# Performance work log

Hardware: AMD Instinct MI355X
Metric: run time of the kernel (lower is better)

Reference implementation:

```python
import jax, jax.numpy as jnp
import numpy as np

N_NODES = 10000
N_EDGES = 320000
D_FEAT = 128          # per-node feature dim -> in_dim = 2*D_FEAT = 256
OUT_DIM = 128
SCALES = 3


def setup_inputs() -> dict:
    key = jax.random.key(0)
    ks = jax.random.split(key, 7)
    node_features = jax.random.normal(ks[0], (N_NODES, D_FEAT), dtype=jnp.float32)
    temporal_info = jax.random.normal(ks[1], (N_NODES,), dtype=jnp.float32)
    in_dim_p1 = 2 * D_FEAT + 1  # 257: concat(src, dest) + temporal gap
    W1 = jax.random.normal(ks[2], (SCALES, in_dim_p1, OUT_DIM), dtype=jnp.float32) * 0.05
    b1 = jax.random.normal(ks[3], (SCALES, OUT_DIM), dtype=jnp.float32) * 0.05
    W2 = jax.random.normal(ks[4], (SCALES, OUT_DIM, OUT_DIM), dtype=jnp.float32) * 0.05
    b2 = jax.random.normal(ks[5], (SCALES, OUT_DIM), dtype=jnp.float32) * 0.05
    edge_index = jax.random.randint(ks[6], (2, N_EDGES), 0, N_NODES, dtype=jnp.int64)
    return {
        "node_features": node_features,
        "temporal_info": temporal_info,
        "W1": W1, "b1": b1, "W2": W2, "b2": b2,
        "edge_index": edge_index,
    }


def reference(node_features, temporal_info, W1, b1, W2, b2, edge_index):
    src, dest = edge_index[0], edge_index[1]
    # gather node pairs + temporal gap -> [E, 2*D+1]
    gap = (temporal_info[src] - temporal_info[dest])[:, None]
    edge_features = jnp.concatenate(
        [node_features[src], node_features[dest], gap], axis=-1)
    # all scales' 2-layer MLPs in one batched einsum; s = scale axis
    h = jax.nn.relu(jnp.einsum('ef,sfo->seo', edge_features, W1) + b1[:, None, :])
    tokens = jnp.einsum('seo,sop->sep', h, W2) + b2[:, None, :]  # [S, E, OUT]
    return tokens.mean(axis=0)  # mean over scales -> [E, OUT]
```

## Files before the change

kernel.cpp:

```cpp
#include <hip/hip_runtime.h>
#include <stdint.h>

#define NN 10000
#define NE 320000
#define DF 128
#define OD 128
#define NS 3

typedef __attribute__((ext_vector_type(8))) short bf16x8;
typedef __attribute__((ext_vector_type(16))) float f32x16;

static __device__ __forceinline__ uint32_t f2bf(float f) {
  uint32_t u = __float_as_uint(f);
  return (u + 0x7FFFu + ((u >> 16) & 1u)) >> 16;
}
static __device__ __forceinline__ float bflo(uint32_t u) { return __uint_as_float(u << 16); }
static __device__ __forceinline__ float bfhi(uint32_t u) { return __uint_as_float(u & 0xFFFF0000u); }

static __device__ __forceinline__ uint32_t relu2(uint32_t a, uint32_t d) {
  float f0 = fmaxf(bflo(a) + bflo(d), 0.0f);
  float f1 = fmaxf(bfhi(a) + bfhi(d), 0.0f);
  return f2bf(f0) | (f2bf(f1) << 16);
}

static __device__ __forceinline__ void lds_barrier() {
  asm volatile("s_waitcnt lgkmcnt(0)" ::: "memory");
  __builtin_amdgcn_s_barrier();
}

__global__ __launch_bounds__(256) void prep_w2(
    const float* __restrict__ W2, const float* __restrict__ b2,
    unsigned short* __restrict__ w2t, float* __restrict__ bmean)
{
  int tid = blockIdx.x * 256 + threadIdx.x;
  if (tid < NS * OD * OD) {
    int s = tid / (OD * OD);
    int r = tid % (OD * OD);
    int k = r / OD;
    int n = r % OD;
    w2t[(s * OD + n) * OD + k] = (unsigned short)f2bf(W2[tid]);
  }
  if (tid < OD) bmean[tid] = (b2[tid] + b2[OD + tid] + b2[2 * OD + tid]) * (1.0f / 3.0f);
}

__global__ __launch_bounds__(256) void node_proj(
    const float* __restrict__ nf, const float* __restrict__ temporal,
    const float* __restrict__ W1, const float* __restrict__ b1,
    unsigned short* __restrict__ Qsrc, unsigned short* __restrict__ Qdst)
{
  __shared__ unsigned short Asm[8 * 64 * 8];
  __shared__ unsigned short Bsm[4 * 8 * 64 * 8];
  __shared__ float tsh[32];

  const int t = threadIdx.x;
  const int c = blockIdx.y;
  const int s = c >> 1, proj = c & 1;

  {
    int o = t & 127, qh = t >> 7;
    const float* wbase = W1 + (size_t)(s * 257 + proj * 128) * OD + o;
    int nt = o >> 5, lnlo = o & 31;
    #pragma unroll
    for (int r = 0; r < 8; r++) {
      int kh = qh * 8 + r;
      float v[8];
      #pragma unroll
      for (int j = 0; j < 8; j++) v[j] = wbase[(size_t)(kh * 8 + j) * OD];
      uint32_t pk[4];
      #pragma unroll
      for (int i = 0; i < 4; i++) pk[i] = f2bf(v[2 * i]) | (f2bf(v[2 * i + 1]) << 16);
      int q = kh >> 1, half = kh & 1;
      uint32_t* d = (uint32_t*)(Bsm + ((nt * 8 + q) * 64 + half * 32 + lnlo) * 8);
      d[0] = pk[0]; d[1] = pk[1]; d[2] = pk[2]; d[3] = pk[3];
    }
  }

  const int lane = t & 63, w = t >> 6;
  const int o = w * 32 + (lane & 31);
  const float w1gv = W1[(size_t)(s * 257 + 256) * OD + o];
  const float b1v = b1[s * OD + o];
  unsigned short* Qt = (proj == 0) ? Qsrc : Qdst;
  const int m = t >> 3, j16 = t & 7;

  for (int it = 0; it < 8; it++) {
    const int m0 = (blockIdx.x * 8 + it) * 32;
    if (m0 >= NN) break;

    if (t < 32) tsh[t] = (m0 + t < NN) ? temporal[m0 + t] : 0.0f;

    {
      int node = m0 + m;
      float v[16];
      if (node < NN) {
        const float4* p = (const float4*)(nf + (size_t)node * DF + j16 * 16);
        #pragma unroll
        for (int i = 0; i < 4; i++) {
          float4 x = p[i];
          v[4 * i] = x.x; v[4 * i + 1] = x.y; v[4 * i + 2] = x.z; v[4 * i + 3] = x.w;
        }
      } else {
        #pragma unroll
        for (int i = 0; i < 16; i++) v[i] = 0.0f;
      }
      uint32_t pk[8];
      #pragma unroll
      for (int i = 0; i < 8; i++) pk[i] = f2bf(v[2 * i]) | (f2bf(v[2 * i + 1]) << 16);
      uint32_t* d0 = (uint32_t*)(Asm + (j16 * 64 + (m ^ j16)) * 8);
      uint32_t* d1 = (uint32_t*)(Asm + (j16 * 64 + ((32 + m) ^ j16)) * 8);
      d0[0] = pk[0]; d0[1] = pk[1]; d0[2] = pk[2]; d0[3] = pk[3];
      d1[0] = pk[4]; d1[1] = pk[5]; d1[2] = pk[6]; d1[3] = pk[7];
    }
    __syncthreads();

    f32x16 C;
    #pragma unroll
    for (int i = 0; i < 16; i++) C[i] = 0.0f;
    #pragma unroll
    for (int q = 0; q < 8; q++) {
      bf16x8 a = *(const bf16x8*)(Asm + (q * 64 + (lane ^ q)) * 8);
      bf16x8 b = *(const bf16x8*)(Bsm + ((w * 8 + q) * 64 + lane) * 8);
      C = __builtin_amdgcn_mfma_f32_32x32x16_bf16(a, b, C, 0, 0, 0);
    }

    #pragma unroll
    for (int r = 0; r < 16; r++) {
      int row = (r & 3) + 8 * (r >> 2) + 4 * (lane >> 5);
      int node = m0 + row;
      if (node < NN) {
        float val = C[r];
        if (proj == 0) val += b1v + tsh[row] * w1gv;
        else           val -= tsh[row] * w1gv;
        Qt[(size_t)node * (NS * OD) + s * OD + o] = (unsigned short)f2bf(val);
      }
    }
    __syncthreads();
  }
}

__global__ __launch_bounds__(256) void edge_mlp(
    const unsigned short* __restrict__ Qsrc, const unsigned short* __restrict__ Qdst,
    const unsigned short* __restrict__ W2T, const float* __restrict__ bmean,
    const int* __restrict__ ei, float* __restrict__ out)
{
  __shared__ unsigned short hsm[NS * 8 * 64 * 8];

  const int t = threadIdx.x;
  const int lane = t & 63, w = t >> 6;
  const int nlo = lane & 31, khi = lane >> 5;

  bf16x8 bfrag[NS][8];
  {
    int n = w * 32 + nlo;
    #pragma unroll
    for (int s = 0; s < NS; s++) {
      const unsigned short* base = W2T + ((s * OD + n) * OD + khi * 8);
      #pragma unroll
      for (int q = 0; q < 8; q++)
        bfrag[s][q] = *(const bf16x8*)(base + q * 16);
    }
  }
  const float bmv = bmean[w * 32 + nlo];

  const int m = t >> 3, j16 = t & 7;

  int sn[4], dn[4];
  #pragma unroll
  for (int tt = 0; tt < 4; tt++) {
    int e = blockIdx.x * 128 + tt * 32 + m;
    sn[tt] = ei[e];
    dn[tt] = ei[NE + e];
  }

  uint4 G[12], G2[12];
  {
    const unsigned short* ps = Qsrc + (size_t)sn[0] * (NS * OD) + j16 * 16;
    const unsigned short* pd = Qdst + (size_t)dn[0] * (NS * OD) + j16 * 16;
    #pragma unroll
    for (int s = 0; s < NS; s++) {
      G[4 * s + 0] = *(const uint4*)(ps + s * OD);
      G[4 * s + 1] = *(const uint4*)(ps + s * OD + 8);
      G[4 * s + 2] = *(const uint4*)(pd + s * OD);
      G[4 * s + 3] = *(const uint4*)(pd + s * OD + 8);
    }
  }

  #pragma unroll
  for (int tt = 0; tt < 4; tt++) {
    const int e0 = blockIdx.x * 128 + tt * 32;

    #pragma unroll
    for (int s = 0; s < NS; s++) {
      uint4 a0 = G[4 * s + 0], a1 = G[4 * s + 1];
      uint4 d0 = G[4 * s + 2], d1 = G[4 * s + 3];
      uint4 w0, w1;
      w0.x = relu2(a0.x, d0.x); w0.y = relu2(a0.y, d0.y);
      w0.z = relu2(a0.z, d0.z); w0.w = relu2(a0.w, d0.w);
      w1.x = relu2(a1.x, d1.x); w1.y = relu2(a1.y, d1.y);
      w1.z = relu2(a1.z, d1.z); w1.w = relu2(a1.w, d1.w);
      *(uint4*)(hsm + ((s * 8 + j16) * 64 + (m ^ j16)) * 8) = w0;
      *(uint4*)(hsm + ((s * 8 + j16) * 64 + ((32 + m) ^ j16)) * 8) = w1;
    }

    if (tt < 3) {
      const unsigned short* ps = Qsrc + (size_t)sn[tt + 1] * (NS * OD) + j16 * 16;
      const unsigned short* pd = Qdst + (size_t)dn[tt + 1] * (NS * OD) + j16 * 16;
      #pragma unroll
      for (int s = 0; s < NS; s++) {
        G2[4 * s + 0] = *(const uint4*)(ps + s * OD);
        G2[4 * s + 1] = *(const uint4*)(ps + s * OD + 8);
        G2[4 * s + 2] = *(const uint4*)(pd + s * OD);
        G2[4 * s + 3] = *(const uint4*)(pd + s * OD + 8);
      }
    }
    lds_barrier();

    f32x16 C;
    #pragma unroll
    for (int i = 0; i < 16; i++) C[i] = 0.0f;
    __builtin_amdgcn_s_setprio(1);
    #pragma unroll
    for (int s = 0; s < NS; s++) {
      #pragma unroll
      for (int q = 0; q < 8; q++) {
        bf16x8 a = *(const bf16x8*)(hsm + ((s * 8 + q) * 64 + (lane ^ q)) * 8);
        C = __builtin_amdgcn_mfma_f32_32x32x16_bf16(a, bfrag[s][q], C, 0, 0, 0);
      }
    }
    __builtin_amdgcn_s_setprio(0);

    #pragma unroll
    for (int r = 0; r < 16; r++) {
      int row = (r & 3) + 8 * (r >> 2) + 4 * khi;
      __builtin_nontemporal_store(C[r] * (1.0f / 3.0f) + bmv,
          &out[(size_t)(e0 + row) * OD + w * 32 + nlo]);
    }
    lds_barrier();

    #pragma unroll
    for (int i = 0; i < 12; i++) G[i] = G2[i];
  }
}

extern "C" void kernel_launch(void* const* d_in, const int* in_sizes, int n_in,
                              void* d_out, int out_size, void* d_ws, size_t ws_size,
                              hipStream_t stream) {
  const float* nf       = (const float*)d_in[0];
  const float* temporal = (const float*)d_in[1];
  const float* W1       = (const float*)d_in[2];
  const float* b1       = (const float*)d_in[3];
  const float* W2       = (const float*)d_in[4];
  const float* b2       = (const float*)d_in[5];
  const int*   ei       = (const int*)d_in[6];
  float* out = (float*)d_out;

  char* ws = (char*)d_ws;
  unsigned short* Qsrc = (unsigned short*)ws;
  unsigned short* Qdst = (unsigned short*)(ws + 7680000);
  unsigned short* W2T  = (unsigned short*)(ws + 15360000);
  float*          bmv  = (float*)(ws + 15360000 + 98304);

  prep_w2 <<<dim3(192),    dim3(256), 0, stream>>>(W2, b2, W2T, bmv);
  node_proj<<<dim3(40, 6), dim3(256), 0, stream>>>(nf, temporal, W1, b1, Qsrc, Qdst);
  edge_mlp <<<dim3(2500),  dim3(256), 0, stream>>>(Qsrc, Qdst, W2T, bmv, ei, out);
}
```

Measured before the change: 267.1 us.

## Reload W2 fragments per tile from fragment-packed layout to raise occupancy

Register-resident W2 fragments (24 bf16x8 per thread) and the double-buffered gather registers are replaced. W2 is now pre-packed into a per-thread fragment order and reloaded from global/L2 on every edge tile with coalesced 16-byte loads. Gathers are issued at the start of each iteration without prefetching, the loop is not unrolled, and launch_bounds requests 4 blocks per CU. The aim is to cut VGPR pressure and raise occupancy so more waves hide gather latency. The cost is repeated W2 traffic from cache and the loss of explicit software prefetch overlap.

Result: slower. 295.8 us (+10.7%).

```diff
diff --git a/kernel.cpp b/kernel.cpp
--- a/kernel.cpp
+++ b/kernel.cpp
@@ -30,17 +30,20 @@
 
 __global__ __launch_bounds__(256) void prep_w2(
     const float* __restrict__ W2, const float* __restrict__ b2,
-    unsigned short* __restrict__ w2t, float* __restrict__ bmean)
+    unsigned short* __restrict__ w2f, float* __restrict__ bmean)
 {
-  int tid = blockIdx.x * 256 + threadIdx.x;
-  if (tid < NS * OD * OD) {
-    int s = tid / (OD * OD);
-    int r = tid % (OD * OD);
-    int k = r / OD;
-    int n = r % OD;
-    w2t[(s * OD + n) * OD + k] = (unsigned short)f2bf(W2[tid]);
-  }
-  if (tid < OD) bmean[tid] = (b2[tid] + b2[OD + tid] + b2[2 * OD + tid]) * (1.0f / 3.0f);
+  int o = blockIdx.x * 256 + threadIdx.x;
+  if (o < NS * 8 * 256 * 8) {
+    int j = o & 7;
+    int t = (o >> 3) & 255;
+    int q = (o >> 11) & 7;
+    int s = o >> 14;
+    int w = t >> 6, lane = t & 63;
+    int n = w * 32 + (lane & 31);
+    int k = q * 16 + (lane >> 5) * 8 + j;
+    w2f[o] = (unsigned short)f2bf(W2[((size_t)s * OD + k) * OD + n]);
+  }
+  if (o < OD) bmean[o] = (b2[o] + b2[OD + o] + b2[2 * OD + o]) * (1.0f / 3.0f);
 }
 
 __global__ __launch_bounds__(256) void node_proj(
@@ -137,9 +140,9 @@
   }
 }
 
-__global__ __launch_bounds__(256) void edge_mlp(
+__global__ __launch_bounds__(256, 4) void edge_mlp(
     const unsigned short* __restrict__ Qsrc, const unsigned short* __restrict__ Qdst,
-    const unsigned short* __restrict__ W2T, const float* __restrict__ bmean,
+    const unsigned short* __restrict__ W2F, const float* __restrict__ bmean,
     const int* __restrict__ ei, float* __restrict__ out)
 {
   __shared__ unsigned short hsm[NS * 8 * 64 * 8];
@@ -147,46 +150,36 @@
   const int t = threadIdx.x;
   const int lane = t & 63, w = t >> 6;
   const int nlo = lane & 31, khi = lane >> 5;
-
-  bf16x8 bfrag[NS][8];
-  {
-    int n = w * 32 + nlo;
-    #pragma unroll
-    for (int s = 0; s < NS; s++) {
-      const unsigned short* base = W2T + ((s * OD + n) * OD + khi * 8);
-      #pragma unroll
-      for (int q = 0; q < 8; q++)
-        bfrag[s][q] = *(const bf16x8*)(base + q * 16);
-    }
-  }
   const float bmv = bmean[w * 32 + nlo];
-
   const int m = t >> 3, j16 = t & 7;
 
-  int sn[4], dn[4];
-  #pragma unroll
-  for (int tt = 0; tt < 4; tt++) {
-    int e = blockIdx.x * 128 + tt * 32 + m;
-    sn[tt] = ei[e];
-    dn[tt] = ei[NE + e];
-  }
-
-  uint4 G[12], G2[12];
-  {
-    const unsigned short* ps = Qsrc + (size_t)sn[0] * (NS * OD) + j16 * 16;
-    const unsigned short* pd = Qdst + (size_t)dn[0] * (NS * OD) + j16 * 16;
-    #pragma unroll
-    for (int s = 0; s < NS; s++) {
-      G[4 * s + 0] = *(const uint4*)(ps + s * OD);
-      G[4 * s + 1] = *(const uint4*)(ps + s * OD + 8);
-      G[4 * s + 2] = *(const uint4*)(pd + s * OD);
-      G[4 * s + 3] = *(const uint4*)(pd + s * OD + 8);
-    }
-  }
-
-  #pragma unroll
+  const unsigned short* pw0 = W2F + (size_t)t * 8;
+
+  int snn = ei[blockIdx.x * 128 + m];
+  int dnn = ei[NE + blockIdx.x * 128 + m];
+
+  #pragma unroll 1
   for (int tt = 0; tt < 4; tt++) {
     const int e0 = blockIdx.x * 128 + tt * 32;
+    const int sn = snn, dn = dnn;
+
+    if (tt < 3) {
+      snn = ei[e0 + 32 + m];
+      dnn = ei[NE + e0 + 32 + m];
+    }
+
+    uint4 G[12];
+    {
+      const unsigned short* ps = Qsrc + (size_t)sn * (NS * OD) + j16 * 16;
+      const unsigned short* pd = Qdst + (size_t)dn * (NS * OD) + j16 * 16;
+      #pragma unroll
+      for (int s = 0; s < NS; s++) {
+        G[4 * s + 0] = *(const uint4*)(ps + s * OD);
+        G[4 * s + 1] = *(const uint4*)(ps + s * OD + 8);
+        G[4 * s + 2] = *(const uint4*)(pd + s * OD);
+        G[4 * s + 3] = *(const uint4*)(pd + s * OD + 8);
+      }
+    }
 
     #pragma unroll
     for (int s = 0; s < NS; s++) {
@@ -201,17 +194,16 @@
       *(uint4*)(hsm + ((s * 8 + j16) * 64 + ((32 + m) ^ j16)) * 8) = w1;
     }
 
-    if (tt < 3) {
-      const unsigned short* ps = Qsrc + (size_t)sn[tt + 1] * (NS * OD) + j16 * 16;
-      const unsigned short* pd = Qdst + (size_t)dn[tt + 1] * (NS * OD) + j16 * 16;
-      #pragma unroll
-      for (int s = 0; s < NS; s++) {
-        G2[4 * s + 0] = *(const uint4*)(ps + s * OD);
-        G2[4 * s + 1] = *(const uint4*)(ps + s * OD + 8);
-        G2[4 * s + 2] = *(const uint4*)(pd + s * OD);
-        G2[4 * s + 3] = *(const uint4*)(pd + s * OD + 8);
-      }
-    }
+    const unsigned short* pw = pw0;
+    asm volatile("" : "+v"(pw));
+    bf16x8 fA[8], fB[8], fC[8];
+    #pragma unroll
+    for (int q = 0; q < 8; q++) fA[q] = *(const bf16x8*)(pw + (0 * 8 + q) * 2048);
+    #pragma unroll
+    for (int q = 0; q < 8; q++) fB[q] = *(const bf16x8*)(pw + (1 * 8 + q) * 2048);
+    #pragma unroll
+    for (int q = 0; q < 8; q++) fC[q] = *(const bf16x8*)(pw + (2 * 8 + q) * 2048);
+
     lds_barrier();
 
     f32x16 C;
@@ -219,12 +211,19 @@
     for (int i = 0; i < 16; i++) C[i] = 0.0f;
     __builtin_amdgcn_s_setprio(1);
     #pragma unroll
-    for (int s = 0; s < NS; s++) {
-      #pragma unroll
-      for (int q = 0; q < 8; q++) {
-        bf16x8 a = *(const bf16x8*)(hsm + ((s * 8 + q) * 64 + (lane ^ q)) * 8);
-        C = __builtin_amdgcn_mfma_f32_32x32x16_bf16(a, bfrag[s][q], C, 0, 0, 0);
-      }
+    for (int q = 0; q < 8; q++) {
+      bf16x8 a = *(const bf16x8*)(hsm + ((0 * 8 + q) * 64 + (lane ^ q)) * 8);
+      C = __builtin_amdgcn_mfma_f32_32x32x16_bf16(a, fA[q], C, 0, 0, 0);
+    }
+    #pragma unroll
+    for (int q = 0; q < 8; q++) {
+      bf16x8 a = *(const bf16x8*)(hsm + ((1 * 8 + q) * 64 + (lane ^ q)) * 8);
+      C = __builtin_amdgcn_mfma_f32_32x32x16_bf16(a, fB[q], C, 0, 0, 0);
+    }
+    #pragma unroll
+    for (int q = 0; q < 8; q++) {
+      bf16x8 a = *(const bf16x8*)(hsm + ((2 * 8 + q) * 64 + (lane ^ q)) * 8);
+      C = __builtin_amdgcn_mfma_f32_32x32x16_bf16(a, fC[q], C, 0, 0, 0);
     }
     __builtin_amdgcn_s_setprio(0);
 
@@ -235,9 +234,6 @@
           &out[(size_t)(e0 + row) * OD + w * 32 + nlo]);
     }
     lds_barrier();
-
-    #pragma unroll
-    for (int i = 0; i < 12; i++) G[i] = G2[i];
   }
 }
 
@@ -256,10 +252,10 @@
   char* ws = (char*)d_ws;
   unsigned short* Qsrc = (unsigned short*)ws;
   unsigned short* Qdst = (unsigned short*)(ws + 7680000);
-  unsigned short* W2T  = (unsigned short*)(ws + 15360000);
+  unsigned short* W2F  = (unsigned short*)(ws + 15360000);
   float*          bmv  = (float*)(ws + 15360000 + 98304);
 
-  prep_w2 <<<dim3(192),    dim3(256), 0, stream>>>(W2, b2, W2T, bmv);
+  prep_w2 <<<dim3(192),    dim3(256), 0, stream>>>(W2, b2, W2F, bmv);
   node_proj<<<dim3(40, 6), dim3(256), 0, stream>>>(nf, temporal, W1, b1, Qsrc, Qdst);
-  edge_mlp <<<dim3(2500),  dim3(256), 0, stream>>>(Qsrc, Qdst, W2T, bmv, ei, out);
-}
+  edge_mlp <<<dim3(2500),  dim3(256), 0, stream>>>(Qsrc, Qdst, W2F, bmv, ei, out);
+}
```
